# Kernel tuning notes

Hardware: AMD Instinct MI355X
Metric: run time of the kernel (lower is better)

Reference implementation:

```python
import jax, jax.numpy as jnp
import numpy as np

C = 96          # num_features
G = 3           # deform / weight groups
K = 9           # 3x3 kernel taps
OFF_CH = G * 3 * K  # 81: offset-conv output channels


def conv3x3(x, w, b=None):
    out = jax.lax.conv_general_dilated(
        x, w, window_strides=(1, 1), padding=((1, 1), (1, 1)),
        dimension_numbers=('NCHW', 'OIHW', 'NCHW'))
    if b is not None:
        out = out + b[None, :, None, None]
    return out


def offset_gen(x):
    o1, o2, m = jnp.split(x, 3, axis=1)
    return jnp.concatenate([o1, o2], axis=1), jax.nn.sigmoid(m)


def dcn(x, offset, mask, w, b):
    # Modulated deformable conv (DCNv2): offset = [y-offsets (G*K ch), x-offsets (G*K ch)]
    N, Cx, H, W = x.shape
    Cg = Cx // G
    GK = G * K
    dy = offset[:, :GK].reshape(N, G, K, H, W)
    dx = offset[:, GK:].reshape(N, G, K, H, W)
    m = mask.reshape(N, G, K, H, W)
    ky = (jnp.arange(K) // 3 - 1).astype(x.dtype)
    kx = (jnp.arange(K) % 3 - 1).astype(x.dtype)
    # sampling positions: p = p0 + kernel_offset + learned_offset (stride 1, pad 1)
    py = dy + jnp.arange(H, dtype=x.dtype)[:, None] + ky[:, None, None]   # [N,G,K,H,W]
    px = dx + jnp.arange(W, dtype=x.dtype) + kx[:, None, None]
    y0 = jnp.floor(py)
    x0 = jnp.floor(px)
    xf = x.reshape(N, G, Cg, H * W)
    gather = jax.vmap(jax.vmap(lambda xg, ig: xg[:, ig]))  # ([Cg,HW],[KHW]) -> [Cg,KHW]
    val = jnp.zeros((N, G, Cg, K, H, W), x.dtype)
    for cy, cx in ((y0, x0), (y0, x0 + 1), (y0 + 1, x0), (y0 + 1, x0 + 1)):
        wgt = (1 - jnp.abs(py - cy)) * (1 - jnp.abs(px - cx))
        valid = (cy >= 0) & (cy <= H - 1) & (cx >= 0) & (cx <= W - 1)
        iy = jnp.clip(cy, 0, H - 1).astype(jnp.int32)
        ix = jnp.clip(cx, 0, W - 1).astype(jnp.int32)
        idx = (iy * W + ix).reshape(N, G, K * H * W)
        g = gather(xf, idx).reshape(N, G, Cg, K, H, W)
        val = val + g * (wgt * valid.astype(x.dtype))[:, :, None]
    val = val * m[:, :, None]                       # modulation
    wg = w.reshape(G, Cx // G, Cg, K)               # grouped weight [G, Cout/G, Cin/G, K]
    out = jnp.einsum('ngckhw,gock->ngohw', val, wg).reshape(N, Cx, H, W)
    return out + b[None, :, None, None]


def setup_inputs() -> dict:
    key = jax.random.key(0)
    ks = jax.random.split(key, 16)
    B, H, W = 2, 128, 128
    d = {
        'X1': jax.random.normal(ks[0], (B, C, H, W), jnp.float32),
        'X2': jax.random.normal(ks[1], (B, C, H, W), jnp.float32),
        'w_bot': jax.random.normal(ks[2], (C, 2 * C, 3, 3), jnp.float32) * 0.02,
    }
    for i in range(4):
        d[f'w_off{i+1}'] = jax.random.normal(ks[3 + i], (OFF_CH, C, 3, 3), jnp.float32) * 0.02
        d[f'w_d{i+1}'] = jax.random.normal(ks[7 + i], (C, C // G, 3, 3), jnp.float32) * 0.05
        d[f'b_d{i+1}'] = jax.random.normal(ks[11 + i], (C,), jnp.float32) * 0.01
    return d


def reference(X1, X2, w_bot, w_off1, w_off2, w_off3, w_off4,
              w_d1, b_d1, w_d2, b_d2, w_d3, b_d3, w_d4, b_d4):
    B, Cx, H, W = X1.shape
    # frames: f0 = cat(X1, X1), f1 = cat(X1, X2) along channels, flattened to (B*2, 2C, H, W)
    feat = jnp.stack([jnp.concatenate([X1, X1], axis=1),
                      jnp.concatenate([X1, X2], axis=1)], axis=1)
    feat = feat.reshape(B * 2, 2 * Cx, H, W)
    feat = conv3x3(feat, w_bot)
    for w_off, w_d, b_d in ((w_off1, w_d1, b_d1), (w_off2, w_d2, b_d2),
                            (w_off3, w_d3, b_d3), (w_off4, w_d4, b_d4)):
        off, m = offset_gen(conv3x3(feat, w_off))
        feat = dcn(feat, off, m, w_d, b_d)
    return feat[1:2]


if __name__ == '__main__':
    out = reference(**setup_inputs())
    print(out.shape)
```

## Files before the change

kernel.cpp:

```cpp
#include <hip/hip_runtime.h>

#define HW 16384
#define W_ 128
#define RSB 130

typedef short short8 __attribute__((ext_vector_type(8)));
typedef float f32x4 __attribute__((ext_vector_type(4)));
typedef unsigned short ushort8v __attribute__((ext_vector_type(8)));

__device__ __forceinline__ float b2f(unsigned short u) {
    return __uint_as_float(((unsigned)u) << 16);
}
__device__ __forceinline__ unsigned short f2b(float f) {
    unsigned u = __float_as_uint(f);
    return (unsigned short)((u + 0x7fffu + ((u >> 16) & 1u)) >> 16);
}

__global__ __launch_bounds__(256) void pack_nhwc(const float* __restrict__ X1,
                                                 const float* __restrict__ X2,
                                                 unsigned short* __restrict__ dst) {
    int i = blockIdx.x * 256 + threadIdx.x;
    int p = i & (HW - 1);
    int cb = i >> 14;
    if (cb >= 24) return;
    int ch = cb * 8;
    int y = p >> 7, x = p & 127;
    ushort8v o;
#pragma unroll
    for (int j = 0; j < 8; ++j) {
        int c = ch + j;
        float v = (c < 96) ? X1[c * HW + p] : X2[(c - 96) * HW + p];
        o[j] = f2b(v);
    }
    *(ushort8v*)(dst + (size_t)((y + 1) * RSB + (x + 1)) * 192 + ch) = o;
}

__global__ __launch_bounds__(256) void prep_all(
    const float* __restrict__ w_bot,
    const float* __restrict__ w_off0, const float* __restrict__ w_off1,
    const float* __restrict__ w_off2, const float* __restrict__ w_off3,
    const float* __restrict__ w_d0, const float* __restrict__ w_d1,
    const float* __restrict__ w_d2, const float* __restrict__ w_d3,
    unsigned short* __restrict__ wBbot, unsigned short* __restrict__ wBoff,
    unsigned short* __restrict__ wdB,  unsigned short* __restrict__ in_nhwc,
    unsigned short* __restrict__ featA, unsigned short* __restrict__ featB) {
    const int region = blockIdx.y;
    const int i = blockIdx.x * 256 + threadIdx.x;
    if (region == 0) {
        if (i >= 165888) return;
        int v = i & 7, lane = (i >> 3) & 63, t = i >> 9;
        int kc = t % 6; t /= 6;
        int tap = t % 9, nt = t / 9;
        int oc = nt * 16 + (lane & 15), cin = kc * 32 + (lane >> 4) * 8 + v;
        wBbot[i] = f2b(oc < 96 ? w_bot[(oc * 192 + cin) * 9 + tap] : 0.f);
    } else if (region <= 4) {
        if (i >= 82944) return;
        const float* w = region == 1 ? w_off0 : region == 2 ? w_off1
                       : region == 3 ? w_off2 : w_off3;
        int v = i & 7, lane = (i >> 3) & 63, t = i >> 9;
        int kc = t % 3; t /= 3;
        int tap = t % 9, nt = t / 9;
        int oc = nt * 16 + (lane & 15), cin = kc * 32 + (lane >> 4) * 8 + v;
        wBoff[(region - 1) * 82944 + i] = f2b(oc < 81 ? w[(oc * 96 + cin) * 9 + tap] : 0.f);
    } else if (region <= 8) {
        if (i >= 27648) return;
        const float* w = region == 5 ? w_d0 : region == 6 ? w_d1
                       : region == 7 ? w_d2 : w_d3;
        int v = i & 7, lane = (i >> 3) & 63, t = i >> 9;
        int nt = t & 1; t >>= 1;
        int tap = t % 9, g = t / 9;
        int oc = nt * 16 + (lane & 15), c = (lane >> 4) * 8 + v;
        wdB[(region - 5) * 27648 + i] = f2b(w[((g * 32 + oc) * 32 + c) * 9 + tap]);
    } else {
        if (i >= 516 * 48) return;
        int bp = i / 48, c8 = i % 48;
        int y, x;
        if (bp < 130)      { y = 0;   x = bp; }
        else if (bp < 260) { y = 129; x = bp - 130; }
        else { int t2 = bp - 260; y = 1 + (t2 >> 1); x = (t2 & 1) ? 129 : 0; }
        size_t pix = (size_t)y * RSB + x;
        ushort8v z = {0, 0, 0, 0, 0, 0, 0, 0};
        if (c8 < 24)      *(ushort8v*)(in_nhwc + pix * 192 + c8 * 8) = z;
        else if (c8 < 36) *(ushort8v*)(featA + pix * 96 + (c8 - 24) * 8) = z;
        else              *(ushort8v*)(featB + pix * 96 + (c8 - 36) * 8) = z;
    }
}

template<int KC, bool FLAT_OUT>
__global__ __launch_bounds__(256) void conv_mfma(const unsigned short* __restrict__ in,
                                                 const unsigned short* __restrict__ wB,
                                                 unsigned short* __restrict__ outb) {
    const int CP = KC * 32;
    const int tid = threadIdx.x;
    const int lane = tid & 63;
    const int wid = tid >> 6;
    const int msub = wid & 1, nh = wid >> 1;
    const int pbase = blockIdx.x * 32 + msub * 16;
    const int p = pbase + (lane & 15);
    const int y = p >> 7, x = p & 127;
    const int klane = lane >> 4;
    const unsigned short* arow = in + (size_t)((y + 1) * RSB + (x + 1)) * CP + klane * 8;
    const unsigned short* wb = wB + (size_t)(nh * 3) * 9 * KC * 512 + lane * 8;

    f32x4 acc0 = {0.f, 0.f, 0.f, 0.f};
    f32x4 acc1 = {0.f, 0.f, 0.f, 0.f};
    f32x4 acc2 = {0.f, 0.f, 0.f, 0.f};

#pragma unroll
    for (int tap = 0; tap < 9; ++tap) {
        const unsigned short* at = arow + ((tap / 3 - 1) * RSB + (tap % 3 - 1)) * CP;
#pragma unroll
        for (int kc = 0; kc < KC; ++kc) {
            short8 a  = *(const short8*)(at + kc * 32);
            short8 b0 = *(const short8*)(wb + ((0 * 9 + tap) * KC + kc) * 512);
            short8 b1 = *(const short8*)(wb + ((1 * 9 + tap) * KC + kc) * 512);
            short8 b2 = *(const short8*)(wb + ((2 * 9 + tap) * KC + kc) * 512);
            acc0 = __builtin_amdgcn_mfma_f32_16x16x32_bf16(a, b0, acc0, 0, 0, 0);
            acc1 = __builtin_amdgcn_mfma_f32_16x16x32_bf16(a, b1, acc1, 0, 0, 0);
            acc2 = __builtin_amdgcn_mfma_f32_16x16x32_bf16(a, b2, acc2, 0, 0, 0);
        }
    }

    const int col = lane & 15;
#pragma unroll
    for (int r = 0; r < 4; ++r) {
        int pr = pbase + klane * 4 + r;
        int yy = pr >> 7, xx = pr & 127;
        size_t base = FLAT_OUT ? (size_t)pr * 96
                               : (size_t)((yy + 1) * RSB + (xx + 1)) * 96;
        outb[base + (nh * 3 + 0) * 16 + col] = f2b(acc0[r]);
        outb[base + (nh * 3 + 1) * 16 + col] = f2b(acc1[r]);
        outb[base + (nh * 3 + 2) * 16 + col] = f2b(acc2[r]);
    }
}

__global__ __launch_bounds__(512) void offdcn_kernel(
    const unsigned short* __restrict__ feat,
    const unsigned short* __restrict__ wBoff,
    const unsigned short* __restrict__ wdB,
    const float* __restrict__ b_d,
    void* __restrict__ outp, int last) {
    __shared__ float s_off[64][97];

    const int tid = threadIdx.x;
    const int lane = tid & 63;
    const int w = tid >> 6;
    const int col = lane & 15, klane = lane >> 4;
    const int pb = ((blockIdx.x & 7) << 5) + (blockIdx.x >> 3);
    const int P0 = pb * 64;

    {
        const int pf = w >> 1, nh = w & 1;
        const int p = P0 + pf * 16 + col;
        const int y = p >> 7, x = p & 127;
        const unsigned short* arow = feat + (size_t)((y + 1) * RSB + (x + 1)) * 96 + klane * 8;
        const unsigned short* wb = wBoff + (size_t)(nh * 3) * 9 * 3 * 512 + lane * 8;

        f32x4 a0 = {0.f, 0.f, 0.f, 0.f};
        f32x4 a1 = {0.f, 0.f, 0.f, 0.f};
        f32x4 a2 = {0.f, 0.f, 0.f, 0.f};
#pragma unroll
        for (int tap = 0; tap < 9; ++tap) {
            const unsigned short* at = arow + ((tap / 3 - 1) * RSB + (tap % 3 - 1)) * 96;
#pragma unroll
            for (int kc = 0; kc < 3; ++kc) {
                short8 a  = *(const short8*)(at + kc * 32);
                short8 b0 = *(const short8*)(wb + ((0 * 9 + tap) * 3 + kc) * 512);
                short8 b1 = *(const short8*)(wb + ((1 * 9 + tap) * 3 + kc) * 512);
                short8 b2 = *(const short8*)(wb + ((2 * 9 + tap) * 3 + kc) * 512);
                a0 = __builtin_amdgcn_mfma_f32_16x16x32_bf16(a, b0, a0, 0, 0, 0);
                a1 = __builtin_amdgcn_mfma_f32_16x16x32_bf16(a, b1, a1, 0, 0, 0);
                a2 = __builtin_amdgcn_mfma_f32_16x16x32_bf16(a, b2, a2, 0, 0, 0);
            }
        }
#pragma unroll
        for (int r = 0; r < 4; ++r) {
            int pl = pf * 16 + klane * 4 + r;
            s_off[pl][nh * 48 + 0 * 16 + col] = a0[r];
            s_off[pl][nh * 48 + 1 * 16 + col] = a1[r];
            s_off[pl][nh * 48 + 2 * 16 + col] = a2[r];
        }
    }
    __syncthreads();

    for (int sidx = w; sidx < 12; sidx += 8) {
        const int pf = sidx & 3, g = sidx >> 2;
        const int p = P0 + pf * 16 + col;
        const int y = p >> 7, x = p & 127;
        const int pl = pf * 16 + col;
        const int coct = klane * 8;

        float dyv[9], dxv[9], mrv[9];
#pragma unroll
        for (int k = 0; k < 9; ++k) {
            dyv[k] = s_off[pl][g * 9 + k];
            dxv[k] = s_off[pl][27 + g * 9 + k];
            mrv[k] = s_off[pl][54 + g * 9 + k];
        }

        const unsigned short* fgc = feat + g * 32 + coct;
        const unsigned short* wb = wdB + (size_t)g * 9 * 2 * 512 + lane * 8;

        f32x4 acc0 = {0.f, 0.f, 0.f, 0.f};
        f32x4 acc1 = {0.f, 0.f, 0.f, 0.f};

#pragma unroll
        for (int k = 0; k < 9; ++k) {
            float m = 1.f / (1.f + __expf(-mrv[k]));

            float py = dyv[k] + (float)y + (float)(k / 3 - 1);
            float px = dxv[k] + (float)x + (float)(k % 3 - 1);
            float y0f = floorf(py), x0f = floorf(px);
            float fy = py - y0f, fx = px - x0f;

            float vy0 = (y0f >= 0.f   && y0f <= 127.f) ? 1.f : 0.f;
            float vy1 = (y0f >= -1.f  && y0f <= 126.f) ? 1.f : 0.f;
            float vx0 = (x0f >= 0.f   && x0f <= 127.f) ? 1.f : 0.f;
            float vx1 = (x0f >= -1.f  && x0f <= 126.f) ? 1.f : 0.f;

            int iy0r = (int)y0f, ix0r = (int)x0f;
            int iy0 = min(max(iy0r, 0), 127);
            int iy1 = min(max(iy0r + 1, 0), 127);
            int ix0 = min(max(ix0r, 0), 127);
            int ix1 = min(max(ix0r + 1, 0), 127);

            float w00 = (1.f - fy) * (1.f - fx) * vy0 * vx0 * m;
            float w01 = (1.f - fy) * fx        * vy0 * vx1 * m;
            float w10 = fy        * (1.f - fx) * vy1 * vx0 * m;
            float w11 = fy        * fx         * vy1 * vx1 * m;

            int r00 = (iy0 + 1) * RSB + ix0 + 1, r01 = (iy0 + 1) * RSB + ix1 + 1;
            int r10 = (iy1 + 1) * RSB + ix0 + 1, r11 = (iy1 + 1) * RSB + ix1 + 1;
            ushort8v v00 = *(const ushort8v*)(fgc + (size_t)r00 * 96);
            ushort8v v01 = *(const ushort8v*)(fgc + (size_t)r01 * 96);
            ushort8v v10 = *(const ushort8v*)(fgc + (size_t)r10 * 96);
            ushort8v v11 = *(const ushort8v*)(fgc + (size_t)r11 * 96);

            short8 a;
#pragma unroll
            for (int j = 0; j < 8; ++j) {
                float val = w00 * b2f(v00[j]) + w01 * b2f(v01[j])
                          + w10 * b2f(v10[j]) + w11 * b2f(v11[j]);
                a[j] = (short)f2b(val);
            }
            short8 b0 = *(const short8*)(wb + (k * 2 + 0) * 512);
            short8 b1 = *(const short8*)(wb + (k * 2 + 1) * 512);
            acc0 = __builtin_amdgcn_mfma_f32_16x16x32_bf16(a, b0, acc0, 0, 0, 0);
            acc1 = __builtin_amdgcn_mfma_f32_16x16x32_bf16(a, b1, acc1, 0, 0, 0);
        }

#pragma unroll
        for (int r = 0; r < 4; ++r) {
            int pr = P0 + pf * 16 + klane * 4 + r;
            int ch0 = g * 32 + col, ch1 = g * 32 + 16 + col;
            float o0 = acc0[r] + b_d[ch0];
            float o1 = acc1[r] + b_d[ch1];
            if (!last) {
                int yy = pr >> 7, xx = pr & 127;
                unsigned short* fo = (unsigned short*)outp;
                size_t base = (size_t)((yy + 1) * RSB + (xx + 1)) * 96;
                fo[base + ch0] = f2b(o0);
                fo[base + ch1] = f2b(o1);
            } else {
                float* fo = (float*)outp;
                fo[(size_t)ch0 * HW + pr] = o0;
                fo[(size_t)ch1 * HW + pr] = o1;
            }
        }
    }
}

extern "C" void kernel_launch(void* const* d_in, const int* in_sizes, int n_in,
                              void* d_out, int out_size, void* d_ws, size_t ws_size,
                              hipStream_t stream) {
    const float* X1    = (const float*)d_in[0];
    const float* X2    = (const float*)d_in[1];
    const float* w_bot = (const float*)d_in[2];
    const float* w_off[4] = {(const float*)d_in[3], (const float*)d_in[6],
                             (const float*)d_in[9], (const float*)d_in[12]};
    const float* w_d[4]   = {(const float*)d_in[4], (const float*)d_in[7],
                             (const float*)d_in[10], (const float*)d_in[13]};
    const float* b_d[4]   = {(const float*)d_in[5], (const float*)d_in[8],
                             (const float*)d_in[11], (const float*)d_in[14]};

    unsigned short* in_nhwc = (unsigned short*)d_ws;
    unsigned short* featA   = in_nhwc + 3244800;
    unsigned short* featB   = featA + 1622400;
    unsigned short* wBbot   = featB + 1622400;
    unsigned short* wBoff   = wBbot + 165888;
    unsigned short* wdB     = wBoff + 4 * 82944;

    prep_all<<<dim3(648, 10), 256, 0, stream>>>(
        w_bot, w_off[0], w_off[1], w_off[2], w_off[3],
        w_d[0], w_d[1], w_d[2], w_d[3],
        wBbot, wBoff, wdB, in_nhwc, featA, featB);
    pack_nhwc<<<1536, 256, 0, stream>>>(X1, X2, in_nhwc);
    conv_mfma<6, false><<<512, 256, 0, stream>>>(in_nhwc, wBbot, featA);

    unsigned short* cur = featA;
    unsigned short* nxt = featB;
    for (int it = 0; it < 4; ++it) {
        void* outp = (it == 3) ? d_out : (void*)nxt;
        offdcn_kernel<<<256, 512, 0, stream>>>(cur, wBoff + it * 82944,
                                               wdB + it * 27648, b_d[it],
                                               outp, it == 3 ? 1 : 0);
        unsigned short* t = cur; cur = nxt; nxt = t;
    }
}
```

Before: 122.9 us.

## Merge input packing into prep kernel and software-pipeline DCN gathers

Folds the NHWC input packing kernel into the weight-prep kernel as one grid-stride launch, which removes a kernel launch. In the deformable conv stage, it first computes all nine taps' bilinear addresses and weights, then issues the feature gathers three taps ahead of the MFMA compute using rotating buffers, so memory latency overlaps with arithmetic. The extra arrays and buffers raise register pressure in a 512-thread kernel, which may cost occupancy.

```diff
diff --git a/kernel.cpp b/kernel.cpp
--- a/kernel.cpp
+++ b/kernel.cpp
@@ -1,7 +1,6 @@
 #include <hip/hip_runtime.h>
 
 #define HW 16384
-#define W_ 128
 #define RSB 130
 
 typedef short short8 __attribute__((ext_vector_type(8)));
@@ -16,81 +15,76 @@
     return (unsigned short)((u + 0x7fffu + ((u >> 16) & 1u)) >> 16);
 }
 
-__global__ __launch_bounds__(256) void pack_nhwc(const float* __restrict__ X1,
-                                                 const float* __restrict__ X2,
-                                                 unsigned short* __restrict__ dst) {
-    int i = blockIdx.x * 256 + threadIdx.x;
-    int p = i & (HW - 1);
-    int cb = i >> 14;
-    if (cb >= 24) return;
-    int ch = cb * 8;
-    int y = p >> 7, x = p & 127;
-    ushort8v o;
-#pragma unroll
-    for (int j = 0; j < 8; ++j) {
-        int c = ch + j;
-        float v = (c < 96) ? X1[c * HW + p] : X2[(c - 96) * HW + p];
-        o[j] = f2b(v);
-    }
-    *(ushort8v*)(dst + (size_t)((y + 1) * RSB + (x + 1)) * 192 + ch) = o;
-}
-
 __global__ __launch_bounds__(256) void prep_all(
+    const float* __restrict__ X1, const float* __restrict__ X2,
     const float* __restrict__ w_bot,
-    const float* __restrict__ w_off0, const float* __restrict__ w_off1,
-    const float* __restrict__ w_off2, const float* __restrict__ w_off3,
-    const float* __restrict__ w_d0, const float* __restrict__ w_d1,
-    const float* __restrict__ w_d2, const float* __restrict__ w_d3,
+    const float* __restrict__ wo0, const float* __restrict__ wo1,
+    const float* __restrict__ wo2, const float* __restrict__ wo3,
+    const float* __restrict__ wd0, const float* __restrict__ wd1,
+    const float* __restrict__ wd2, const float* __restrict__ wd3,
     unsigned short* __restrict__ wBbot, unsigned short* __restrict__ wBoff,
     unsigned short* __restrict__ wdB,  unsigned short* __restrict__ in_nhwc,
     unsigned short* __restrict__ featA, unsigned short* __restrict__ featB) {
-    const int region = blockIdx.y;
-    const int i = blockIdx.x * 256 + threadIdx.x;
-    if (region == 0) {
-        if (i >= 165888) return;
-        int v = i & 7, lane = (i >> 3) & 63, t = i >> 9;
-        int kc = t % 6; t /= 6;
-        int tap = t % 9, nt = t / 9;
-        int oc = nt * 16 + (lane & 15), cin = kc * 32 + (lane >> 4) * 8 + v;
-        wBbot[i] = f2b(oc < 96 ? w_bot[(oc * 192 + cin) * 9 + tap] : 0.f);
-    } else if (region <= 4) {
-        if (i >= 82944) return;
-        const float* w = region == 1 ? w_off0 : region == 2 ? w_off1
-                       : region == 3 ? w_off2 : w_off3;
-        int v = i & 7, lane = (i >> 3) & 63, t = i >> 9;
-        int kc = t % 3; t /= 3;
-        int tap = t % 9, nt = t / 9;
-        int oc = nt * 16 + (lane & 15), cin = kc * 32 + (lane >> 4) * 8 + v;
-        wBoff[(region - 1) * 82944 + i] = f2b(oc < 81 ? w[(oc * 96 + cin) * 9 + tap] : 0.f);
-    } else if (region <= 8) {
-        if (i >= 27648) return;
-        const float* w = region == 5 ? w_d0 : region == 6 ? w_d1
-                       : region == 7 ? w_d2 : w_d3;
-        int v = i & 7, lane = (i >> 3) & 63, t = i >> 9;
-        int nt = t & 1; t >>= 1;
-        int tap = t % 9, g = t / 9;
-        int oc = nt * 16 + (lane & 15), c = (lane >> 4) * 8 + v;
-        wdB[(region - 5) * 27648 + i] = f2b(w[((g * 32 + oc) * 32 + c) * 9 + tap]);
-    } else {
-        if (i >= 516 * 48) return;
-        int bp = i / 48, c8 = i % 48;
-        int y, x;
-        if (bp < 130)      { y = 0;   x = bp; }
-        else if (bp < 260) { y = 129; x = bp - 130; }
-        else { int t2 = bp - 260; y = 1 + (t2 >> 1); x = (t2 & 1) ? 129 : 0; }
-        size_t pix = (size_t)y * RSB + x;
-        ushort8v z = {0, 0, 0, 0, 0, 0, 0, 0};
-        if (c8 < 24)      *(ushort8v*)(in_nhwc + pix * 192 + c8 * 8) = z;
-        else if (c8 < 36) *(ushort8v*)(featA + pix * 96 + (c8 - 24) * 8) = z;
-        else              *(ushort8v*)(featB + pix * 96 + (c8 - 36) * 8) = z;
-    }
-}
-
-template<int KC, bool FLAT_OUT>
-__global__ __launch_bounds__(256) void conv_mfma(const unsigned short* __restrict__ in,
-                                                 const unsigned short* __restrict__ wB,
-                                                 unsigned short* __restrict__ outb) {
-    const int CP = KC * 32;
+    const int N0 = 165888, N1 = N0 + 331776, N2 = N1 + 110592,
+              N3 = N2 + 393216, N4 = N3 + 24768;
+    for (int idx = blockIdx.x * 256 + threadIdx.x; idx < N4; idx += 131072) {
+        if (idx < N0) {
+            int i = idx;
+            int v = i & 7, lane = (i >> 3) & 63, t = i >> 9;
+            int kc = t % 6; t /= 6;
+            int tap = t % 9, nt = t / 9;
+            int oc = nt * 16 + (lane & 15), cin = kc * 32 + (lane >> 4) * 8 + v;
+            wBbot[i] = f2b(oc < 96 ? w_bot[(oc * 192 + cin) * 9 + tap] : 0.f);
+        } else if (idx < N1) {
+            int j = idx - N0;
+            int l = j / 82944, i = j - l * 82944;
+            const float* w = l == 0 ? wo0 : l == 1 ? wo1 : l == 2 ? wo2 : wo3;
+            int v = i & 7, lane = (i >> 3) & 63, t = i >> 9;
+            int kc = t % 3; t /= 3;
+            int tap = t % 9, nt = t / 9;
+            int oc = nt * 16 + (lane & 15), cin = kc * 32 + (lane >> 4) * 8 + v;
+            wBoff[j] = f2b(oc < 81 ? w[(oc * 96 + cin) * 9 + tap] : 0.f);
+        } else if (idx < N2) {
+            int j = idx - N1;
+            int l = j / 27648, i = j - l * 27648;
+            const float* w = l == 0 ? wd0 : l == 1 ? wd1 : l == 2 ? wd2 : wd3;
+            int v = i & 7, lane = (i >> 3) & 63, t = i >> 9;
+            int nt = t & 1; t >>= 1;
+            int tap = t % 9, g = t / 9;
+            int oc = nt * 16 + (lane & 15), c = (lane >> 4) * 8 + v;
+            wdB[j] = f2b(w[((g * 32 + oc) * 32 + c) * 9 + tap]);
+        } else if (idx < N3) {
+            int j = idx - N2;
+            int cb = j >> 14, p = j & (HW - 1);
+            int ch = cb * 8;
+            int y = p >> 7, x = p & 127;
+            ushort8v o;
+#pragma unroll
+            for (int q = 0; q < 8; ++q) {
+                int c = ch + q;
+                float v = (c < 96) ? X1[c * HW + p] : X2[(c - 96) * HW + p];
+                o[q] = f2b(v);
+            }
+            *(ushort8v*)(in_nhwc + (size_t)((y + 1) * RSB + (x + 1)) * 192 + ch) = o;
+        } else {
+            int j = idx - N3;
+            int bp = j / 48, c8 = j - bp * 48;
+            int y, x;
+            if (bp < 130)      { y = 0;   x = bp; }
+            else if (bp < 260) { y = 129; x = bp - 130; }
+            else { int t2 = bp - 260; y = 1 + (t2 >> 1); x = (t2 & 1) ? 129 : 0; }
+            size_t pix = (size_t)y * RSB + x;
+            ushort8v z = {0, 0, 0, 0, 0, 0, 0, 0};
+            if (c8 < 24)      *(ushort8v*)(in_nhwc + pix * 192 + c8 * 8) = z;
+            else if (c8 < 36) *(ushort8v*)(featA + pix * 96 + (c8 - 24) * 8) = z;
+            else              *(ushort8v*)(featB + pix * 96 + (c8 - 36) * 8) = z;
+        }
+    }
+}
+
+__global__ __launch_bounds__(256) void conv_bot(const unsigned short* __restrict__ in,
+                                                const unsigned short* __restrict__ wB,
+                                                unsigned short* __restrict__ outb) {
     const int tid = threadIdx.x;
     const int lane = tid & 63;
     const int wid = tid >> 6;
@@ -99,38 +93,35 @@
     const int p = pbase + (lane & 15);
     const int y = p >> 7, x = p & 127;
     const int klane = lane >> 4;
-    const unsigned short* arow = in + (size_t)((y + 1) * RSB + (x + 1)) * CP + klane * 8;
-    const unsigned short* wb = wB + (size_t)(nh * 3) * 9 * KC * 512 + lane * 8;
-
-    f32x4 acc0 = {0.f, 0.f, 0.f, 0.f};
-    f32x4 acc1 = {0.f, 0.f, 0.f, 0.f};
-    f32x4 acc2 = {0.f, 0.f, 0.f, 0.f};
-
+    const unsigned short* arow = in + (size_t)((y + 1) * RSB + (x + 1)) * 192 + klane * 8;
+    const unsigned short* wb = wB + (size_t)(nh * 3) * 9 * 6 * 512 + lane * 8;
+
+    f32x4 a0 = {0.f, 0.f, 0.f, 0.f};
+    f32x4 a1 = {0.f, 0.f, 0.f, 0.f};
+    f32x4 a2 = {0.f, 0.f, 0.f, 0.f};
 #pragma unroll
     for (int tap = 0; tap < 9; ++tap) {
-        const unsigned short* at = arow + ((tap / 3 - 1) * RSB + (tap % 3 - 1)) * CP;
-#pragma unroll
-        for (int kc = 0; kc < KC; ++kc) {
+        const unsigned short* at = arow + ((tap / 3 - 1) * RSB + (tap % 3 - 1)) * 192;
+#pragma unroll
+        for (int kc = 0; kc < 6; ++kc) {
             short8 a  = *(const short8*)(at + kc * 32);
-            short8 b0 = *(const short8*)(wb + ((0 * 9 + tap) * KC + kc) * 512);
-            short8 b1 = *(const short8*)(wb + ((1 * 9 + tap) * KC + kc) * 512);
-            short8 b2 = *(const short8*)(wb + ((2 * 9 + tap) * KC + kc) * 512);
-            acc0 = __builtin_amdgcn_mfma_f32_16x16x32_bf16(a, b0, acc0, 0, 0, 0);
-            acc1 = __builtin_amdgcn_mfma_f32_16x16x32_bf16(a, b1, acc1, 0, 0, 0);
-            acc2 = __builtin_amdgcn_mfma_f32_16x16x32_bf16(a, b2, acc2, 0, 0, 0);
-        }
-    }
-
+            short8 b0 = *(const short8*)(wb + ((0 * 9 + tap) * 6 + kc) * 512);
+            short8 b1 = *(const short8*)(wb + ((1 * 9 + tap) * 6 + kc) * 512);
+            short8 b2 = *(const short8*)(wb + ((2 * 9 + tap) * 6 + kc) * 512);
+            a0 = __builtin_amdgcn_mfma_f32_16x16x32_bf16(a, b0, a0, 0, 0, 0);
+            a1 = __builtin_amdgcn_mfma_f32_16x16x32_bf16(a, b1, a1, 0, 0, 0);
+            a2 = __builtin_amdgcn_mfma_f32_16x16x32_bf16(a, b2, a2, 0, 0, 0);
+        }
+    }
     const int col = lane & 15;
 #pragma unroll
     for (int r = 0; r < 4; ++r) {
         int pr = pbase + klane * 4 + r;
         int yy = pr >> 7, xx = pr & 127;
-        size_t base = FLAT_OUT ? (size_t)pr * 96
-                               : (size_t)((yy + 1) * RSB + (xx + 1)) * 96;
-        outb[base + (nh * 3 + 0) * 16 + col] = f2b(acc0[r]);
-        outb[base + (nh * 3 + 1) * 16 + col] = f2b(acc1[r]);
-        outb[base + (nh * 3 + 2) * 16 + col] = f2b(acc2[r]);
+        size_t base = (size_t)((yy + 1) * RSB + (xx + 1)) * 96;
+        outb[base + (nh * 3 + 0) * 16 + col] = f2b(a0[r]);
+        outb[base + (nh * 3 + 1) * 16 + col] = f2b(a1[r]);
+        outb[base + (nh * 3 + 2) * 16 + col] = f2b(a2[r]);
     }
 }
 
@@ -190,26 +181,20 @@
         const int pl = pf * 16 + col;
         const int coct = klane * 8;
 
-        float dyv[9], dxv[9], mrv[9];
-#pragma unroll
-        for (int k = 0; k < 9; ++k) {
-            dyv[k] = s_off[pl][g * 9 + k];
-            dxv[k] = s_off[pl][27 + g * 9 + k];
-            mrv[k] = s_off[pl][54 + g * 9 + k];
-        }
-
         const unsigned short* fgc = feat + g * 32 + coct;
         const unsigned short* wb = wdB + (size_t)g * 9 * 2 * 512 + lane * 8;
 
-        f32x4 acc0 = {0.f, 0.f, 0.f, 0.f};
-        f32x4 acc1 = {0.f, 0.f, 0.f, 0.f};
-
+        int adr[9][4];
+        float wgt[9][4];
 #pragma unroll
         for (int k = 0; k < 9; ++k) {
-            float m = 1.f / (1.f + __expf(-mrv[k]));
-
-            float py = dyv[k] + (float)y + (float)(k / 3 - 1);
-            float px = dxv[k] + (float)x + (float)(k % 3 - 1);
+            float dy = s_off[pl][g * 9 + k];
+            float dx = s_off[pl][27 + g * 9 + k];
+            float mr = s_off[pl][54 + g * 9 + k];
+            float m = 1.f / (1.f + __expf(-mr));
+
+            float py = dy + (float)y + (float)(k / 3 - 1);
+            float px = dx + (float)x + (float)(k % 3 - 1);
             float y0f = floorf(py), x0f = floorf(px);
             float fy = py - y0f, fx = px - x0f;
 
@@ -224,30 +209,47 @@
             int ix0 = min(max(ix0r, 0), 127);
             int ix1 = min(max(ix0r + 1, 0), 127);
 
-            float w00 = (1.f - fy) * (1.f - fx) * vy0 * vx0 * m;
-            float w01 = (1.f - fy) * fx        * vy0 * vx1 * m;
-            float w10 = fy        * (1.f - fx) * vy1 * vx0 * m;
-            float w11 = fy        * fx         * vy1 * vx1 * m;
-
-            int r00 = (iy0 + 1) * RSB + ix0 + 1, r01 = (iy0 + 1) * RSB + ix1 + 1;
-            int r10 = (iy1 + 1) * RSB + ix0 + 1, r11 = (iy1 + 1) * RSB + ix1 + 1;
-            ushort8v v00 = *(const ushort8v*)(fgc + (size_t)r00 * 96);
-            ushort8v v01 = *(const ushort8v*)(fgc + (size_t)r01 * 96);
-            ushort8v v10 = *(const ushort8v*)(fgc + (size_t)r10 * 96);
-            ushort8v v11 = *(const ushort8v*)(fgc + (size_t)r11 * 96);
-
-            short8 a;
-#pragma unroll
-            for (int j = 0; j < 8; ++j) {
-                float val = w00 * b2f(v00[j]) + w01 * b2f(v01[j])
-                          + w10 * b2f(v10[j]) + w11 * b2f(v11[j]);
-                a[j] = (short)f2b(val);
-            }
-            short8 b0 = *(const short8*)(wb + (k * 2 + 0) * 512);
-            short8 b1 = *(const short8*)(wb + (k * 2 + 1) * 512);
-            acc0 = __builtin_amdgcn_mfma_f32_16x16x32_bf16(a, b0, acc0, 0, 0, 0);
-            acc1 = __builtin_amdgcn_mfma_f32_16x16x32_bf16(a, b1, acc1, 0, 0, 0);
-        }
+            wgt[k][0] = (1.f - fy) * (1.f - fx) * vy0 * vx0 * m;
+            wgt[k][1] = (1.f - fy) * fx        * vy0 * vx1 * m;
+            wgt[k][2] = fy        * (1.f - fx) * vy1 * vx0 * m;
+            wgt[k][3] = fy        * fx         * vy1 * vx1 * m;
+
+            adr[k][0] = (iy0 + 1) * RSB + ix0 + 1;
+            adr[k][1] = (iy0 + 1) * RSB + ix1 + 1;
+            adr[k][2] = (iy1 + 1) * RSB + ix0 + 1;
+            adr[k][3] = (iy1 + 1) * RSB + ix1 + 1;
+        }
+
+        f32x4 acc0 = {0.f, 0.f, 0.f, 0.f};
+        f32x4 acc1 = {0.f, 0.f, 0.f, 0.f};
+
+        ushort8v ga[4], gb[4], gc[4];
+#define LDG(buf, kk) { \
+        buf[0] = *(const ushort8v*)(fgc + (size_t)adr[kk][0] * 96); \
+        buf[1] = *(const ushort8v*)(fgc + (size_t)adr[kk][1] * 96); \
+        buf[2] = *(const ushort8v*)(fgc + (size_t)adr[kk][2] * 96); \
+        buf[3] = *(const ushort8v*)(fgc + (size_t)adr[kk][3] * 96); }
+#define CMP(buf, kk) { \
+        short8 a; \
+        _Pragma("unroll") for (int j = 0; j < 8; ++j) { \
+            float val = wgt[kk][0] * b2f(buf[0][j]) + wgt[kk][1] * b2f(buf[1][j]) \
+                      + wgt[kk][2] * b2f(buf[2][j]) + wgt[kk][3] * b2f(buf[3][j]); \
+            a[j] = (short)f2b(val); } \
+        short8 b0 = *(const short8*)(wb + ((kk) * 2 + 0) * 512); \
+        short8 b1 = *(const short8*)(wb + ((kk) * 2 + 1) * 512); \
+        acc0 = __builtin_amdgcn_mfma_f32_16x16x32_bf16(a, b0, acc0, 0, 0, 0); \
+        acc1 = __builtin_amdgcn_mfma_f32_16x16x32_bf16(a, b1, acc1, 0, 0, 0); }
+
+        LDG(ga, 0); LDG(gb, 1); LDG(gc, 2);
+        CMP(ga, 0); LDG(ga, 3);
+        CMP(gb, 1); LDG(gb, 4);
+        CMP(gc, 2); LDG(gc, 5);
+        CMP(ga, 3); LDG(ga, 6);
+        CMP(gb, 4); LDG(gb, 7);
+        CMP(gc, 5); LDG(gc, 8);
+        CMP(ga, 6); CMP(gb, 7); CMP(gc, 8);
+#undef LDG
+#undef CMP
 
 #pragma unroll
         for (int r = 0; r < 4; ++r) {
@@ -276,12 +278,12 @@
     const float* X1    = (const float*)d_in[0];
     const float* X2    = (const float*)d_in[1];
     const float* w_bot = (const float*)d_in[2];
-    const float* w_off[4] = {(const float*)d_in[3], (const float*)d_in[6],
-                             (const float*)d_in[9], (const float*)d_in[12]};
-    const float* w_d[4]   = {(const float*)d_in[4], (const float*)d_in[7],
-                             (const float*)d_in[10], (const float*)d_in[13]};
-    const float* b_d[4]   = {(const float*)d_in[5], (const float*)d_in[8],
-                             (const float*)d_in[11], (const float*)d_in[14]};
+    const float* wo0 = (const float*)d_in[3],  *wo1 = (const float*)d_in[6],
+               *wo2 = (const float*)d_in[9],  *wo3 = (const float*)d_in[12];
+    const float* wd0 = (const float*)d_in[4],  *wd1 = (const float*)d_in[7],
+               *wd2 = (const float*)d_in[10], *wd3 = (const float*)d_in[13];
+    const float* bd[4] = {(const float*)d_in[5], (const float*)d_in[8],
+                          (const float*)d_in[11], (const float*)d_in[14]};
 
     unsigned short* in_nhwc = (unsigned short*)d_ws;
     unsigned short* featA   = in_nhwc + 3244800;
@@ -290,19 +292,17 @@
     unsigned short* wBoff   = wBbot + 165888;
     unsigned short* wdB     = wBoff + 4 * 82944;
 
-    prep_all<<<dim3(648, 10), 256, 0, stream>>>(
-        w_bot, w_off[0], w_off[1], w_off[2], w_off[3],
-        w_d[0], w_d[1], w_d[2], w_d[3],
-        wBbot, wBoff, wdB, in_nhwc, featA, featB);
-    pack_nhwc<<<1536, 256, 0, stream>>>(X1, X2, in_nhwc);
-    conv_mfma<6, false><<<512, 256, 0, stream>>>(in_nhwc, wBbot, featA);
+    prep_all<<<512, 256, 0, stream>>>(X1, X2, w_bot, wo0, wo1, wo2, wo3,
+                                      wd0, wd1, wd2, wd3,
+                                      wBbot, wBoff, wdB, in_nhwc, featA, featB);
+    conv_bot<<<512, 256, 0, stream>>>(in_nhwc, wBbot, featA);
 
     unsigned short* cur = featA;
     unsigned short* nxt = featB;
     for (int it = 0; it < 4; ++it) {
         void* outp = (it == 3) ? d_out : (void*)nxt;
         offdcn_kernel<<<256, 512, 0, stream>>>(cur, wBoff + it * 82944,
-                                               wdB + it * 27648, b_d[it],
+                                               wdB + it * 27648, bd[it],
                                                outp, it == 3 ? 1 : 0);
         unsigned short* t = cur; cur = nxt; nxt = t;
     }
```

Measured after the change: 119.0 us. 3.2% less time.
